# Performance work log

Hardware: AMD Instinct MI355X
Metric: run time of the kernel (lower is better)

Reference implementation:

```python
import jax, jax.numpy as jnp
import numpy as np

B, N, D, H = 32, 64, 64, 4
E = 4 * D
HD = E // H
EPS = 1e-10
TAU = 1.0


def _ln(x, g, b, eps=1e-5):
    m = x.mean(-1, keepdims=True)
    v = ((x - m) ** 2).mean(-1, keepdims=True)
    return (x - m) * jax.lax.rsqrt(v + eps) * g + b


def setup_inputs() -> dict:
    key = jax.random.key(0)
    ks = jax.random.split(key, 8)
    x = jax.random.normal(ks[0], (B, N, D), jnp.float32)
    A = jax.random.normal(ks[1], (B, N, N, 2 * D), jnp.float32)
    attn_mask = jax.random.randint(ks[2], (B, N, N), 0, 2).astype(jnp.int32)
    gumbel_u = jax.random.uniform(ks[3], (B, N, H, N), jnp.float32, minval=1e-6, maxval=1.0)
    in_proj_w = (jax.random.normal(ks[4], (3 * E, E), jnp.float32) * (E ** -0.5))
    in_proj_b = jnp.zeros((3 * E,), jnp.float32)
    w1 = jax.random.normal(ks[5], (HD, HD), jnp.float32) * (HD ** -0.5)
    b1 = jnp.zeros((HD,), jnp.float32)
    w2 = jax.random.normal(ks[6], (1, HD), jnp.float32) * (HD ** -0.5)
    b2 = jnp.zeros((1,), jnp.float32)
    return dict(x=x, A=A, attn_mask=attn_mask, gumbel_u=gumbel_u,
                ln_node_g=jnp.ones((D,), jnp.float32), ln_node_b=jnp.zeros((D,), jnp.float32),
                ln_edge_g=jnp.ones((2 * D,), jnp.float32), ln_edge_b=jnp.zeros((2 * D,), jnp.float32),
                in_proj_w=in_proj_w, in_proj_b=in_proj_b, w1=w1, b1=b1, w2=w2, b2=b2)


def reference(x, A, attn_mask, gumbel_u, ln_node_g, ln_node_b, ln_edge_g, ln_edge_b,
              in_proj_w, in_proj_b, w1, b1, w2, b2):
    b, n, d = x.shape
    e = 4 * d
    hd = e // H
    mask = attn_mask.astype(x.dtype)                      # (b, target, neighbor), 1/0
    ped = (mask.sum(-1) > 0).astype(x.dtype)[..., None]   # (b, n, 1)
    xn = _ln(x, ln_node_g, ln_node_b) * ped
    An = _ln(A, ln_edge_g, ln_edge_b) * jnp.transpose(mask, (0, 2, 1))[..., None]
    # broadcast concat: (b, neighbor, target, 4d)
    xneigh = jnp.broadcast_to(xn[:, :, None, :], (b, n, n, d))
    xtarg = jnp.broadcast_to(xn[:, None, :, :], (b, n, n, d))
    A4 = jnp.concatenate([xneigh, xtarg, An], axis=-1)
    Ap = jnp.transpose(A4, (0, 2, 1, 3))                  # (b, target, neighbor, 4d)
    # in-projection (torch MHA layout: rows [q; k; v])
    qkv = jnp.einsum('btme,fe->btmf', Ap, in_proj_w) + in_proj_b
    q, k, v = jnp.split(qkv, 3, axis=-1)
    q = q.reshape(b, n, n, H, hd) * (hd ** -0.5)
    k = k.reshape(b, n, n, H, hd)
    v = v.reshape(b, n, n, H, hd)
    scores = jnp.einsum('btjhd,btkhd->bthjk', q, k)       # per-target neighborhood attention
    m3 = mask[:, :, :, None] * mask[:, :, None, :]        # (b, t, j, k)
    w = jax.nn.softmax(scores, axis=-1) * m3[:, :, None, :, :]
    w = w / (w.sum(-1, keepdims=True) + EPS)
    A2 = jnp.einsum('bthjk,btkhd->bthjd', w, v)           # (b, target, head, neighbor, hd)
    hmid = jax.nn.relu(jnp.einsum('bthjd,od->bthjo', A2, w1) + b1)
    logits = (jnp.einsum('bthjo,xo->bthjx', hmid, w2) + b2)[..., 0]  # (b, t, h, j)
    em = jax.nn.softmax(logits, axis=-1) * mask[:, :, None, :]
    em = em / (em.sum(-1, keepdims=True) + EPS)
    g = -jnp.log(-jnp.log(gumbel_u + EPS) + EPS)
    sampled = jax.nn.softmax((jnp.log(em + EPS) + g) / TAU, axis=-1)
    return em, sampled
```

## Files before the change

kernel.cpp:

```cpp
#include <hip/hip_runtime.h>
#include <hip/hip_bf16.h>
#include <math.h>


typedef __attribute__((ext_vector_type(8))) short short8;
typedef __attribute__((ext_vector_type(4))) short short4v;
typedef __attribute__((ext_vector_type(4))) float f32x4;

__device__ __forceinline__ short f2b(float f) {
  return (short)__builtin_bit_cast(unsigned short, __float2bfloat16(f));
}

#define WCS 136
#define TS  72

#define OFF_K0  18432
#define OFF_VT0 36864
#define OFF_F   55296
#define LDS_BYTES 59904

__global__ __launch_bounds__(256) void k_node_ln(
    const float* __restrict__ x, const int* __restrict__ mask,
    const float* __restrict__ g, const float* __restrict__ bb,
    float* __restrict__ xn) {
  int tid = threadIdx.x;
  int row = blockIdx.x * 4 + (tid >> 6);
  int lane = tid & 63;
  float v = x[row * 64 + lane];
  float s = v;
#pragma unroll
  for (int m = 1; m < 64; m <<= 1) s += __shfl_xor(s, m, 64);
  float mean = s * (1.0f / 64.0f);
  float dv = v - mean;
  float s2 = dv * dv;
#pragma unroll
  for (int m = 1; m < 64; m <<= 1) s2 += __shfl_xor(s2, m, 64);
  float rstd = rsqrtf(s2 * (1.0f / 64.0f) + 1e-5f);
  float msum = (float)mask[row * 64 + lane];
#pragma unroll
  for (int m = 1; m < 64; m <<= 1) msum += __shfl_xor(msum, m, 64);
  float ped = (msum > 0.0f) ? 1.0f : 0.0f;
  xn[row * 64 + lane] = (dv * rstd * g[lane] + bb[lane]) * ped;
}

__global__ __launch_bounds__(256) void k_t12(
    const float* __restrict__ xn, const float* __restrict__ W,
    const float* __restrict__ bias, float* __restrict__ T1s, float* __restrict__ T2) {
  __shared__ __align__(16) float sx[8 * 64];
  int tid = threadIdx.x;
  int r0 = blockIdx.x * 8;
#pragma unroll
  for (int u = 0; u < 2; ++u) {
    int idx = tid + 256 * u;
    sx[idx] = xn[r0 * 64 + idx];
  }
  __syncthreads();
#pragma unroll
  for (int ff = 0; ff < 3; ++ff) {
    int f = tid + 256 * ff;
    float acc1[8], acc2[8];
#pragma unroll
    for (int r = 0; r < 8; ++r) { acc1[r] = 0.f; acc2[r] = 0.f; }
    for (int e4 = 0; e4 < 64; e4 += 4) {
      float4 wa = *(const float4*)&W[f * 256 + e4];
      float4 wb = *(const float4*)&W[f * 256 + 64 + e4];
#pragma unroll
      for (int r = 0; r < 8; ++r) {
        float4 xv = *(const float4*)&sx[r * 64 + e4];
        acc1[r] += wa.x * xv.x + wa.y * xv.y + wa.z * xv.z + wa.w * xv.w;
        acc2[r] += wb.x * xv.x + wb.y * xv.y + wb.z * xv.z + wb.w * xv.w;
      }
    }
    float bv = bias[f];
    int p = f >> 8, hh = (f >> 6) & 3, dcol = f & 63;
#pragma unroll
    for (int r = 0; r < 8; ++r) {
      int m = r0 + r;
      int bb2 = m >> 6, mm = m & 63;
      int wv_ = mm >> 4;
      int lane, reg;
      if (p < 2) {
        lane = ((dcol >> 2) & 3) * 16 + (mm & 15);
        reg = (dcol >> 4) * 4 + (dcol & 3);
      } else {
        lane = ((mm >> 2) & 3) * 16 + (dcol & 15);
        reg = (dcol >> 4) * 4 + (mm & 3);
      }
      T1s[(size_t)((((bb2 * 3 + p) * 4 + hh) * 4 + wv_) * 64 + lane) * 16 + reg] =
          acc1[r];
      T2[m * 768 + f] = acc2[r] + bv;
    }
  }
}

__global__ __launch_bounds__(256) void k_wb(const float* __restrict__ W,
                                            const float* __restrict__ w1,
                                            short* __restrict__ Wb,
                                            short* __restrict__ w1b) {
  int idx = blockIdx.x * 256 + threadIdx.x;
  if (idx < 12288) {
    int f = idx >> 4, gi = idx & 15;
    const float* src = &W[(size_t)f * 256 + 128 + gi * 8];
    short8 o;
#pragma unroll
    for (int i = 0; i < 8; ++i) o[i] = f2b(src[i]);
    *(short8*)&Wb[f * 128 + gi * 8] = o;
  } else if (idx < 12288 + 512) {
    int g2 = idx - 12288;
    int f = g2 >> 3, gi = g2 & 7;
    const float* src = &w1[f * 64 + gi * 8];
    short8 o;
#pragma unroll
    for (int i = 0; i < 8; ++i) o[i] = f2b(src[i]);
    *(short8*)&w1b[f * 64 + gi * 8] = o;
  }
}

__global__ __launch_bounds__(256, 2) void k_main(
    const float* __restrict__ A, const int* __restrict__ mask,
    const float* __restrict__ gu, const float* __restrict__ leg,
    const float* __restrict__ leb, const float* __restrict__ b1g,
    const float* __restrict__ w2g, const float* __restrict__ b2g,
    const float* __restrict__ T1s, const float* __restrict__ T2,
    const short* __restrict__ Wb, const short* __restrict__ w1b,
    float* __restrict__ out) {
  __shared__ __align__(16) unsigned char smem[LDS_BYTES];
  short* sWc = (short*)smem;
  float* sF  = (float*)(smem + OFF_F);

  int tid = threadIdx.x;
  int bid0 = blockIdx.x;
  int wg = (bid0 & 7) * 128 + (bid0 >> 3);
  int tq = wg & 31, b = wg >> 5;
  int t0 = tq * 2;
  int bt0 = b * 64 + t0;
  int wave = tid >> 6, lane = tid & 63, lr = lane & 15, lh = lane >> 4;

  if (tid < 64) sF[384 + tid] = (float)mask[bt0 * 64 + tid];
  else if (tid < 128) sF[448 + tid - 64] = (float)mask[(bt0 + 1) * 64 + tid - 64];
  else if (tid < 192) sF[512 + tid - 128] = b1g[tid - 128];
  else sF[576 + tid - 192] = w2g[tid - 192];

  short8 af[2][4];
  {
    int m0 = wave * 16 + lr;
    float4 a4[2][8];
    float mean[2], rstd[2], mv[2];
#pragma unroll
    for (int e = 0; e < 2; ++e) {
      const float* Ar = A + ((size_t)((b * 64 + m0) * 64 + t0 + e)) * 128;
#pragma unroll
      for (int ks = 0; ks < 4; ++ks) {
        a4[e][2 * ks]     = *(const float4*)&Ar[ks * 32 + lh * 8];
        a4[e][2 * ks + 1] = *(const float4*)&Ar[ks * 32 + lh * 8 + 4];
      }
      float s = 0.f, s2 = 0.f;
#pragma unroll
      for (int q = 0; q < 8; ++q) {
        float4 u0 = a4[e][q];
        s += u0.x + u0.y + u0.z + u0.w;
        s2 += u0.x * u0.x + u0.y * u0.y + u0.z * u0.z + u0.w * u0.w;
      }
      s += __shfl_xor(s, 16, 64);  s += __shfl_xor(s, 32, 64);
      s2 += __shfl_xor(s2, 16, 64); s2 += __shfl_xor(s2, 32, 64);
      mean[e] = s * (1.0f / 128.0f);
      float var = s2 * (1.0f / 128.0f) - mean[e] * mean[e];
      rstd[e] = rsqrtf(var + 1e-5f);
      mv[e] = (float)mask[(bt0 + e) * 64 + m0];
    }
#pragma unroll
    for (int ks = 0; ks < 4; ++ks) {
      float4 g0 = *(const float4*)&leg[ks * 32 + lh * 8];
      float4 g1 = *(const float4*)&leg[ks * 32 + lh * 8 + 4];
      float4 c0 = *(const float4*)&leb[ks * 32 + lh * 8];
      float4 c1 = *(const float4*)&leb[ks * 32 + lh * 8 + 4];
      float gg[8] = {g0.x, g0.y, g0.z, g0.w, g1.x, g1.y, g1.z, g1.w};
      float cc[8] = {c0.x, c0.y, c0.z, c0.w, c1.x, c1.y, c1.z, c1.w};
#pragma unroll
      for (int e = 0; e < 2; ++e) {
        float4 u0 = a4[e][2 * ks], u1 = a4[e][2 * ks + 1];
        float vv[8] = {u0.x, u0.y, u0.z, u0.w, u1.x, u1.y, u1.z, u1.w};
#pragma unroll
        for (int i = 0; i < 8; ++i)
          af[e][ks][i] = f2b(((vv[i] - mean[e]) * rstd[e] * gg[i] + cc[i]) * mv[e]);
      }
    }
  }

#pragma unroll 1
  for (int h = 0; h < 4; ++h) {
    __syncthreads();
    if (tid < 192) sF[tid] = T2[bt0 * 768 + (tid >> 6) * 256 + h * 64 + (tid & 63)];
    if (tid >= 64) {
      int i2 = tid - 64;
      sF[192 + i2] = T2[(bt0 + 1) * 768 + (i2 >> 6) * 256 + h * 64 + (i2 & 63)];
    }

#pragma unroll
    for (int pp = 0; pp < 3; ++pp) {
      const int p = (pp + 1) % 3;
      const int Fbase = p * 256 + h * 64;
#pragma unroll
      for (int u = 0; u < 4; ++u) {
        int idx = tid + 256 * u;
        int dR = idx >> 4, gi = idx & 15;
        *(short8*)&sWc[dR * WCS + gi * 8] =
            *(const short8*)&Wb[(size_t)(Fbase + dR) * 128 + gi * 8];
      }
      float4 t1f[4];
#pragma unroll
      for (int nt = 0; nt < 4; ++nt)
        t1f[nt] = *(const float4*)&T1s[
            (size_t)((((b * 3 + p) * 4 + h) * 4 + wave) * 64 + lane) * 16 + nt * 4];
      __syncthreads();
      f32x4 acc0[4], acc1[4];
#pragma unroll
      for (int nt = 0; nt < 4; ++nt) {
        acc0[nt][0] = t1f[nt].x; acc0[nt][1] = t1f[nt].y;
        acc0[nt][2] = t1f[nt].z; acc0[nt][3] = t1f[nt].w;
        acc1[nt] = acc0[nt];
      }
      if (p == 2) {
#pragma unroll
        for (int ks = 0; ks < 4; ++ks)
#pragma unroll
          for (int nt = 0; nt < 4; ++nt) {
            short8 bf = *(const short8*)&sWc[(nt * 16 + lr) * WCS + ks * 32 + lh * 8];
            acc0[nt] = __builtin_amdgcn_mfma_f32_16x16x32_bf16(af[0][ks], bf, acc0[nt], 0, 0, 0);
            acc1[nt] = __builtin_amdgcn_mfma_f32_16x16x32_bf16(af[1][ks], bf, acc1[nt], 0, 0, 0);
          }
      } else {
#pragma unroll
        for (int ks = 0; ks < 4; ++ks)
#pragma unroll
          for (int nt = 0; nt < 4; ++nt) {
            short8 bf = *(const short8*)&sWc[(nt * 16 + lr) * WCS + ks * 32 + lh * 8];
            acc0[nt] = __builtin_amdgcn_mfma_f32_16x16x32_bf16(bf, af[0][ks], acc0[nt], 0, 0, 0);
            acc1[nt] = __builtin_amdgcn_mfma_f32_16x16x32_bf16(bf, af[1][ks], acc1[nt], 0, 0, 0);
          }
      }
      if (p == 0) __syncthreads();
#pragma unroll
      for (int e = 0; e < 2; ++e) {
        const f32x4* acc = (e == 0) ? acc0 : acc1;
        if (p == 2) {
          short* sVTt = (short*)(smem + OFF_VT0 + e * 9216);
#pragma unroll
          for (int nt = 0; nt < 4; ++nt) {
            float t2v = sF[e * 192 + 128 + nt * 16 + lr];
            short4v vp;
#pragma unroll
            for (int r = 0; r < 4; ++r) vp[r] = f2b(acc[nt][r] + t2v);
            *(short4v*)&sVTt[(nt * 16 + lr) * TS + wave * 16 + lh * 4] = vp;
          }
        } else {
          float scale = (p == 0) ? 0.125f : 1.0f;
          short* dst = (p == 0) ? (short*)(smem + e * 9216)
                                : (short*)(smem + OFF_K0 + e * 9216);
#pragma unroll
          for (int nt = 0; nt < 4; ++nt) {
            float4 t24 = *(const float4*)&sF[e * 192 + p * 64 + nt * 16 + lh * 4];
            float tv[4] = {t24.x, t24.y, t24.z, t24.w};
            short4v qp;
#pragma unroll
            for (int r = 0; r < 4; ++r) qp[r] = f2b((acc[nt][r] + tv[r]) * scale);
            *(short4v*)&dst[(wave * 16 + lr) * TS + nt * 16 + lh * 4] = qp;
          }
        }
      }
      if (p != 0) __syncthreads();
    }

#pragma unroll
    for (int e = 0; e < 2; ++e) {
      short* sQt = (short*)(smem + e * 9216);
      short* sKt = (short*)(smem + OFF_K0 + e * 9216);
      f32x4 sc[4] = {};
#pragma unroll
      for (int ks = 0; ks < 2; ++ks) {
        short8 qf = *(const short8*)&sQt[(wave * 16 + lr) * TS + ks * 32 + lh * 8];
#pragma unroll
        for (int nt = 0; nt < 4; ++nt) {
          short8 kf = *(const short8*)&sKt[(nt * 16 + lr) * TS + ks * 32 + lh * 8];
          sc[nt] = __builtin_amdgcn_mfma_f32_16x16x32_bf16(kf, qf, sc[nt], 0, 0, 0);
        }
      }
      float mj = sF[384 + e * 64 + wave * 16 + lr];
      float mx = sc[0][0];
#pragma unroll
      for (int nt = 0; nt < 4; ++nt)
#pragma unroll
        for (int r = 0; r < 4; ++r) mx = fmaxf(mx, sc[nt][r]);
      mx = fmaxf(mx, __shfl_xor(mx, 16, 64));
      mx = fmaxf(mx, __shfl_xor(mx, 32, 64));
      float pv[4][4], mkv[4][4], Zf = 0.f, S = 0.f;
#pragma unroll
      for (int nt = 0; nt < 4; ++nt) {
        float4 mk4 = *(const float4*)&sF[384 + e * 64 + nt * 16 + lh * 4];
        float mk[4] = {mk4.x, mk4.y, mk4.z, mk4.w};
#pragma unroll
        for (int r = 0; r < 4; ++r) {
          float ev = __expf(sc[nt][r] - mx);
          pv[nt][r] = ev;
          mkv[nt][r] = mk[r];
          Zf += ev;
          S += ev * mk[r];
        }
      }
      Zf += __shfl_xor(Zf, 16, 64); Zf += __shfl_xor(Zf, 32, 64);
      S  += __shfl_xor(S, 16, 64);  S  += __shfl_xor(S, 32, 64);
      float inv = mj / (S + 1e-10f * Zf);
#pragma unroll
      for (int nt = 0; nt < 4; ++nt) {
        short4v wp;
#pragma unroll
        for (int r = 0; r < 4; ++r) wp[r] = f2b(pv[nt][r] * mkv[nt][r] * inv);
        *(short4v*)&sQt[(wave * 16 + lr) * TS + nt * 16 + lh * 4] = wp;
      }
    }
    __syncthreads();

#pragma unroll
    for (int e = 0; e < 2; ++e) {
      short* sWtt = (short*)(smem + e * 9216);
      short* sVTt = (short*)(smem + OFF_VT0 + e * 9216);
      short* sA2t = (short*)(smem + OFF_K0 + e * 9216);
      f32x4 a2[4] = {};
#pragma unroll
      for (int ks = 0; ks < 2; ++ks) {
        short8 wf = *(const short8*)&sWtt[(wave * 16 + lr) * TS + ks * 32 + lh * 8];
#pragma unroll
        for (int nt = 0; nt < 4; ++nt) {
          short8 vf = *(const short8*)&sVTt[(nt * 16 + lr) * TS + ks * 32 + lh * 8];
          a2[nt] = __builtin_amdgcn_mfma_f32_16x16x32_bf16(vf, wf, a2[nt], 0, 0, 0);
        }
      }
#pragma unroll
      for (int nt = 0; nt < 4; ++nt) {
        short4v ap;
#pragma unroll
        for (int r = 0; r < 4; ++r) ap[r] = f2b(a2[nt][r]);
        *(short4v*)&sA2t[(wave * 16 + lr) * TS + nt * 16 + lh * 4] = ap;
      }
      f32x4 hm[4] = {};
#pragma unroll
      for (int ks = 0; ks < 2; ++ks) {
        short8 a2f = *(const short8*)&sA2t[(wave * 16 + lr) * TS + ks * 32 + lh * 8];
#pragma unroll
        for (int nt = 0; nt < 4; ++nt) {
          short8 wf = *(const short8*)&w1b[(nt * 16 + lr) * 64 + ks * 32 + lh * 8];
          hm[nt] = __builtin_amdgcn_mfma_f32_16x16x32_bf16(wf, a2f, hm[nt], 0, 0, 0);
        }
      }
      float pp_ = 0.f;
#pragma unroll
      for (int nt = 0; nt < 4; ++nt) {
        float4 b14 = *(const float4*)&sF[512 + nt * 16 + lh * 4];
        float4 w24 = *(const float4*)&sF[576 + nt * 16 + lh * 4];
        float bb4[4] = {b14.x, b14.y, b14.z, b14.w};
        float ww4[4] = {w24.x, w24.y, w24.z, w24.w};
#pragma unroll
        for (int r = 0; r < 4; ++r)
          pp_ += fmaxf(hm[nt][r] + bb4[r], 0.f) * ww4[r];
      }
      pp_ += __shfl_xor(pp_, 16, 64);
      pp_ += __shfl_xor(pp_, 32, 64);
      if (lh == 0) sF[640 + (e * 4 + h) * 64 + wave * 16 + lr] = pp_;
    }
  }
  __syncthreads();

#pragma unroll
  for (int it = 0; it < 2; ++it) {
    int tile = it, hh = wave, j = lane;
    int btx = bt0 + tile;
    float l = sF[640 + (tile * 4 + hh) * 64 + j] + b2g[0];
    float mjv = sF[384 + tile * 64 + j];
    float mx = l;
#pragma unroll
    for (int mm = 1; mm < 64; mm <<= 1) mx = fmaxf(mx, __shfl_xor(mx, mm, 64));
    float pv = __expf(l - mx);
    float Z = pv;
#pragma unroll
    for (int mm = 1; mm < 64; mm <<= 1) Z += __shfl_xor(Z, mm, 64);
    float ep = (pv / Z) * mjv;
    float S = ep;
#pragma unroll
    for (int mm = 1; mm < 64; mm <<= 1) S += __shfl_xor(S, mm, 64);
    float em = ep / (S + 1e-10f);
    float u = gu[((size_t)btx * 4 + hh) * 64 + j];
    float gg = -__logf(-__logf(u + 1e-10f) + 1e-10f);
    float l2 = __logf(em + 1e-10f) + gg;
    float mx2 = l2;
#pragma unroll
    for (int mm = 1; mm < 64; mm <<= 1) mx2 = fmaxf(mx2, __shfl_xor(mx2, mm, 64));
    float p2 = __expf(l2 - mx2);
    float Z2 = p2;
#pragma unroll
    for (int mm = 1; mm < 64; mm <<= 1) Z2 += __shfl_xor(Z2, mm, 64);
    float smp = p2 / Z2;
    size_t o = ((size_t)btx * 4 + hh) * 64 + j;
    out[o] = em;
    out[524288 + o] = smp;
  }
}

extern "C" void kernel_launch(void* const* d_in, const int* in_sizes, int n_in,
                              void* d_out, int out_size, void* d_ws, size_t ws_size,
                              hipStream_t stream) {
  const float* x    = (const float*)d_in[0];
  const float* A    = (const float*)d_in[1];
  const int*   mask = (const int*)d_in[2];
  const float* gu   = (const float*)d_in[3];
  const float* lng  = (const float*)d_in[4];
  const float* lnb  = (const float*)d_in[5];
  const float* leg  = (const float*)d_in[6];
  const float* leb  = (const float*)d_in[7];
  const float* W    = (const float*)d_in[8];
  const float* bias = (const float*)d_in[9];
  const float* w1   = (const float*)d_in[10];
  const float* b1   = (const float*)d_in[11];
  const float* w2   = (const float*)d_in[12];
  const float* b2   = (const float*)d_in[13];
  float* out = (float*)d_out;
  float* ws  = (float*)d_ws;

  float* xn  = ws;
  float* T1s = xn + 131072;
  float* T2  = T1s + 1572864;
  short* Wb  = (short*)(T2 + 1572864);
  short* w1b = Wb + 98304;

  k_wb<<<50, 256, 0, stream>>>(W, w1, Wb, w1b);
  k_node_ln<<<512, 256, 0, stream>>>(x, mask, lng, lnb, xn);
  k_t12<<<256, 256, 0, stream>>>(xn, W, bias, T1s, T2);
  k_main<<<1024, 256, 0, stream>>>(A, mask, gu, leg, leb, b1, w2, b2,
                                   T1s, T2, Wb, w1b, out);
}
```

Before: 119.0 us.

## Shrink LDS footprint, read T2/mask from global, interleave per-head output softmax

After: 231.8 us. 1.95x slower.

```diff
diff --git a/kernel.cpp b/kernel.cpp
--- a/kernel.cpp
+++ b/kernel.cpp
@@ -12,12 +12,12 @@
 }
 
 #define WCS 136
-#define TS  72
-
-#define OFF_K0  18432
-#define OFF_VT0 36864
-#define OFF_F   55296
-#define LDS_BYTES 59904
+#define TS  68
+
+#define OFF_K0  17408
+#define OFF_VT0 34816
+#define OFF_F   52224
+#define LDS_BYTES 53248
 
 __global__ __launch_bounds__(256) void k_node_ln(
     const float* __restrict__ x, const int* __restrict__ mask,
@@ -81,10 +81,10 @@
       int lane, reg;
       if (p < 2) {
         lane = ((dcol >> 2) & 3) * 16 + (mm & 15);
-        reg = (dcol >> 4) * 4 + (dcol & 3);
+        reg  = (dcol >> 4) * 4 + (dcol & 3);
       } else {
         lane = ((mm >> 2) & 3) * 16 + (dcol & 15);
-        reg = (dcol >> 4) * 4 + (mm & 3);
+        reg  = (dcol >> 4) * 4 + (mm & 3);
       }
       T1s[(size_t)((((bb2 * 3 + p) * 4 + hh) * 4 + wv_) * 64 + lane) * 16 + reg] =
           acc1[r];
@@ -116,7 +116,7 @@
   }
 }
 
-__global__ __launch_bounds__(256, 2) void k_main(
+__global__ __launch_bounds__(256) void k_main(
     const float* __restrict__ A, const int* __restrict__ mask,
     const float* __restrict__ gu, const float* __restrict__ leg,
     const float* __restrict__ leb, const float* __restrict__ b1g,
@@ -125,8 +125,8 @@
     const short* __restrict__ Wb, const short* __restrict__ w1b,
     float* __restrict__ out) {
   __shared__ __align__(16) unsigned char smem[LDS_BYTES];
-  short* sWc = (short*)smem;
-  float* sF  = (float*)(smem + OFF_F);
+  short* sWc  = (short*)smem;
+  float* sLog = (float*)(smem + OFF_F);
 
   int tid = threadIdx.x;
   int bid0 = blockIdx.x;
@@ -135,11 +135,9 @@
   int t0 = tq * 2;
   int bt0 = b * 64 + t0;
   int wave = tid >> 6, lane = tid & 63, lr = lane & 15, lh = lane >> 4;
-
-  if (tid < 64) sF[384 + tid] = (float)mask[bt0 * 64 + tid];
-  else if (tid < 128) sF[448 + tid - 64] = (float)mask[(bt0 + 1) * 64 + tid - 64];
-  else if (tid < 192) sF[512 + tid - 128] = b1g[tid - 128];
-  else sF[576 + tid - 192] = w2g[tid - 192];
+  float b2v = b2g[0];
+  const float* T2r[2] = {T2 + (size_t)bt0 * 768, T2 + (size_t)(bt0 + 1) * 768};
+  const int* mrow[2] = {mask + bt0 * 64, mask + (bt0 + 1) * 64};
 
   short8 af[2][4];
   {
@@ -166,7 +164,7 @@
       mean[e] = s * (1.0f / 128.0f);
       float var = s2 * (1.0f / 128.0f) - mean[e] * mean[e];
       rstd[e] = rsqrtf(var + 1e-5f);
-      mv[e] = (float)mask[(bt0 + e) * 64 + m0];
+      mv[e] = (float)mrow[e][m0];
     }
 #pragma unroll
     for (int ks = 0; ks < 4; ++ks) {
@@ -190,10 +188,37 @@
 #pragma unroll 1
   for (int h = 0; h < 4; ++h) {
     __syncthreads();
-    if (tid < 192) sF[tid] = T2[bt0 * 768 + (tid >> 6) * 256 + h * 64 + (tid & 63)];
-    if (tid >= 64) {
-      int i2 = tid - 64;
-      sF[192 + i2] = T2[(bt0 + 1) * 768 + (i2 >> 6) * 256 + h * 64 + (i2 & 63)];
+
+    if (h > 0 && wave < 2) {
+      int hh = h - 1, tile = wave, btx = bt0 + tile, j = lane;
+      float l = sLog[((hh & 1) * 2 + tile) * 64 + j] + b2v;
+      float mjv = (float)mask[btx * 64 + j];
+      float mx = l;
+#pragma unroll
+      for (int mm = 1; mm < 64; mm <<= 1) mx = fmaxf(mx, __shfl_xor(mx, mm, 64));
+      float pv = __expf(l - mx);
+      float Z = pv;
+#pragma unroll
+      for (int mm = 1; mm < 64; mm <<= 1) Z += __shfl_xor(Z, mm, 64);
+      float ep = (pv / Z) * mjv;
+      float S = ep;
+#pragma unroll
+      for (int mm = 1; mm < 64; mm <<= 1) S += __shfl_xor(S, mm, 64);
+      float em = ep / (S + 1e-10f);
+      float u = gu[((size_t)btx * 4 + hh) * 64 + j];
+      float gg = -__logf(-__logf(u + 1e-10f) + 1e-10f);
+      float l2 = __logf(em + 1e-10f) + gg;
+      float mx2 = l2;
+#pragma unroll
+      for (int mm = 1; mm < 64; mm <<= 1) mx2 = fmaxf(mx2, __shfl_xor(mx2, mm, 64));
+      float p2 = __expf(l2 - mx2);
+      float Z2 = p2;
+#pragma unroll
+      for (int mm = 1; mm < 64; mm <<= 1) Z2 += __shfl_xor(Z2, mm, 64);
+      float smp = p2 / Z2;
+      size_t o = ((size_t)btx * 4 + hh) * 64 + j;
+      out[o] = em;
+      out[524288 + o] = smp;
     }
 
 #pragma unroll
@@ -212,6 +237,21 @@
       for (int nt = 0; nt < 4; ++nt)
         t1f[nt] = *(const float4*)&T1s[
             (size_t)((((b * 3 + p) * 4 + h) * 4 + wave) * 64 + lane) * 16 + nt * 4];
+      float4 t2f[2][4];
+      float t2sv[2][4];
+      if (p == 2) {
+#pragma unroll
+        for (int e = 0; e < 2; ++e)
+#pragma unroll
+          for (int nt = 0; nt < 4; ++nt)
+            t2sv[e][nt] = T2r[e][512 + h * 64 + nt * 16 + lr];
+      } else {
+#pragma unroll
+        for (int e = 0; e < 2; ++e)
+#pragma unroll
+          for (int nt = 0; nt < 4; ++nt)
+            t2f[e][nt] = *(const float4*)&T2r[e][Fbase + nt * 16 + lh * 4];
+      }
       __syncthreads();
       f32x4 acc0[4], acc1[4];
 #pragma unroll
@@ -244,10 +284,10 @@
       for (int e = 0; e < 2; ++e) {
         const f32x4* acc = (e == 0) ? acc0 : acc1;
         if (p == 2) {
-          short* sVTt = (short*)(smem + OFF_VT0 + e * 9216);
+          short* sVTt = (short*)(smem + OFF_VT0 + e * 8704);
 #pragma unroll
           for (int nt = 0; nt < 4; ++nt) {
-            float t2v = sF[e * 192 + 128 + nt * 16 + lr];
+            float t2v = t2sv[e][nt];
             short4v vp;
 #pragma unroll
             for (int r = 0; r < 4; ++r) vp[r] = f2b(acc[nt][r] + t2v);
@@ -255,12 +295,11 @@
           }
         } else {
           float scale = (p == 0) ? 0.125f : 1.0f;
-          short* dst = (p == 0) ? (short*)(smem + e * 9216)
-                                : (short*)(smem + OFF_K0 + e * 9216);
+          short* dst = (p == 0) ? (short*)(smem + e * 8704)
+                                : (short*)(smem + OFF_K0 + e * 8704);
 #pragma unroll
           for (int nt = 0; nt < 4; ++nt) {
-            float4 t24 = *(const float4*)&sF[e * 192 + p * 64 + nt * 16 + lh * 4];
-            float tv[4] = {t24.x, t24.y, t24.z, t24.w};
+            float tv[4] = {t2f[e][nt].x, t2f[e][nt].y, t2f[e][nt].z, t2f[e][nt].w};
             short4v qp;
 #pragma unroll
             for (int r = 0; r < 4; ++r) qp[r] = f2b((acc[nt][r] + tv[r]) * scale);
@@ -273,19 +312,19 @@
 
 #pragma unroll
     for (int e = 0; e < 2; ++e) {
-      short* sQt = (short*)(smem + e * 9216);
-      short* sKt = (short*)(smem + OFF_K0 + e * 9216);
+      short* sQt = (short*)(smem + e * 8704);
+      short* sKt = (short*)(smem + OFF_K0 + e * 8704);
       f32x4 sc[4] = {};
 #pragma unroll
       for (int ks = 0; ks < 2; ++ks) {
-        short8 qf = *(const short8*)&sQt[(wave * 16 + lr) * TS + ks * 32 + lh * 8];
+        short8 qfr = *(const short8*)&sQt[(wave * 16 + lr) * TS + ks * 32 + lh * 8];
 #pragma unroll
         for (int nt = 0; nt < 4; ++nt) {
           short8 kf = *(const short8*)&sKt[(nt * 16 + lr) * TS + ks * 32 + lh * 8];
-          sc[nt] = __builtin_amdgcn_mfma_f32_16x16x32_bf16(kf, qf, sc[nt], 0, 0, 0);
+          sc[nt] = __builtin_amdgcn_mfma_f32_16x16x32_bf16(kf, qfr, sc[nt], 0, 0, 0);
         }
       }
-      float mj = sF[384 + e * 64 + wave * 16 + lr];
+      float mj = (float)mrow[e][wave * 16 + lr];
       float mx = sc[0][0];
 #pragma unroll
       for (int nt = 0; nt < 4; ++nt)
@@ -296,8 +335,8 @@
       float pv[4][4], mkv[4][4], Zf = 0.f, S = 0.f;
 #pragma unroll
       for (int nt = 0; nt < 4; ++nt) {
-        float4 mk4 = *(const float4*)&sF[384 + e * 64 + nt * 16 + lh * 4];
-        float mk[4] = {mk4.x, mk4.y, mk4.z, mk4.w};
+        int4 m4 = *(const int4*)&mrow[e][nt * 16 + lh * 4];
+        float mk[4] = {(float)m4.x, (float)m4.y, (float)m4.z, (float)m4.w};
 #pragma unroll
         for (int r = 0; r < 4; ++r) {
           float ev = __expf(sc[nt][r] - mx);
@@ -322,17 +361,17 @@
 
 #pragma unroll
     for (int e = 0; e < 2; ++e) {
-      short* sWtt = (short*)(smem + e * 9216);
-      short* sVTt = (short*)(smem + OFF_VT0 + e * 9216);
-      short* sA2t = (short*)(smem + OFF_K0 + e * 9216);
+      short* sWtt = (short*)(smem + e * 8704);
+      short* sVTt = (short*)(smem + OFF_VT0 + e * 8704);
+      short* sA2t = (short*)(smem + OFF_K0 + e * 8704);
       f32x4 a2[4] = {};
 #pragma unroll
       for (int ks = 0; ks < 2; ++ks) {
-        short8 wf = *(const short8*)&sWtt[(wave * 16 + lr) * TS + ks * 32 + lh * 8];
+        short8 wfr = *(const short8*)&sWtt[(wave * 16 + lr) * TS + ks * 32 + lh * 8];
 #pragma unroll
         for (int nt = 0; nt < 4; ++nt) {
           short8 vf = *(const short8*)&sVTt[(nt * 16 + lr) * TS + ks * 32 + lh * 8];
-          a2[nt] = __builtin_amdgcn_mfma_f32_16x16x32_bf16(vf, wf, a2[nt], 0, 0, 0);
+          a2[nt] = __builtin_amdgcn_mfma_f32_16x16x32_bf16(vf, wfr, a2[nt], 0, 0, 0);
         }
       }
 #pragma unroll
@@ -348,15 +387,15 @@
         short8 a2f = *(const short8*)&sA2t[(wave * 16 + lr) * TS + ks * 32 + lh * 8];
 #pragma unroll
         for (int nt = 0; nt < 4; ++nt) {
-          short8 wf = *(const short8*)&w1b[(nt * 16 + lr) * 64 + ks * 32 + lh * 8];
-          hm[nt] = __builtin_amdgcn_mfma_f32_16x16x32_bf16(wf, a2f, hm[nt], 0, 0, 0);
+          short8 wf1 = *(const short8*)&w1b[(nt * 16 + lr) * 64 + ks * 32 + lh * 8];
+          hm[nt] = __builtin_amdgcn_mfma_f32_16x16x32_bf16(wf1, a2f, hm[nt], 0, 0, 0);
         }
       }
       float pp_ = 0.f;
 #pragma unroll
       for (int nt = 0; nt < 4; ++nt) {
-        float4 b14 = *(const float4*)&sF[512 + nt * 16 + lh * 4];
-        float4 w24 = *(const float4*)&sF[576 + nt * 16 + lh * 4];
+        float4 b14 = *(const float4*)&b1g[nt * 16 + lh * 4];
+        float4 w24 = *(const float4*)&w2g[nt * 16 + lh * 4];
         float bb4[4] = {b14.x, b14.y, b14.z, b14.w};
         float ww4[4] = {w24.x, w24.y, w24.z, w24.w};
 #pragma unroll
@@ -365,17 +404,15 @@
       }
       pp_ += __shfl_xor(pp_, 16, 64);
       pp_ += __shfl_xor(pp_, 32, 64);
-      if (lh == 0) sF[640 + (e * 4 + h) * 64 + wave * 16 + lr] = pp_;
+      if (lh == 0) sLog[((h & 1) * 2 + e) * 64 + wave * 16 + lr] = pp_;
     }
   }
   __syncthreads();
 
-#pragma unroll
-  for (int it = 0; it < 2; ++it) {
-    int tile = it, hh = wave, j = lane;
-    int btx = bt0 + tile;
-    float l = sF[640 + (tile * 4 + hh) * 64 + j] + b2g[0];
-    float mjv = sF[384 + tile * 64 + j];
+  if (wave < 2) {
+    int hh = 3, tile = wave, btx = bt0 + tile, j = lane;
+    float l = sLog[((hh & 1) * 2 + tile) * 64 + j] + b2v;
+    float mjv = (float)mask[btx * 64 + j];
     float mx = l;
 #pragma unroll
     for (int mm = 1; mm < 64; mm <<= 1) mx = fmaxf(mx, __shfl_xor(mx, mm, 64));
```
